# Kernel optimization log

Measured on AMD Instinct MI355X. Metric: run time of the kernel, lower is better.

## Reference

```python
import jax, jax.numpy as jnp
import numpy as np

N = 20000      # nodes
E = 320000     # edges (avg degree 16)
S = 2          # extra feature axis (mean-pooled before fc)
IN = 128       # in_feats
H = 246        # n_hidden (must be 246 to match fc = Linear(246, 1))


def setup_inputs() -> dict:
    key = jax.random.key(0)
    ks = jax.random.split(key, 8)
    feat = jax.random.normal(ks[0], (N, S, IN), jnp.float32)
    src = jax.random.randint(ks[1], (E,), 0, N, jnp.int32)
    dst = jax.random.randint(ks[2], (E,), 0, N, jnp.int32)
    glorot = lambda k, shp, fan: jax.random.normal(k, shp, jnp.float32) / np.sqrt(fan).astype(np.float32)
    return {
        "features": feat,
        "src": src,
        "dst": dst,
        "W0": glorot(ks[3], (IN, H), IN), "b0": jnp.zeros((H,), jnp.float32),
        "W1": glorot(ks[4], (H, H), H),   "b1": jnp.zeros((H,), jnp.float32),
        "W2": glorot(ks[5], (H, H), H),   "b2": jnp.zeros((H,), jnp.float32),
        "fc_w": glorot(ks[6], (H, 1), H), "fc_b": jnp.zeros((1,), jnp.float32),
    }


def reference(features, src, dst, W0, b0, W1, b1, W2, b2, fc_w, fc_b):
    # DGL GraphConv, norm='both': h' = act( D_in^{-1/2} A D_out^{-1/2} h W + b )
    ones = jnp.ones((src.shape[0],), jnp.float32)
    out_deg = jax.ops.segment_sum(ones, src, num_segments=N)
    in_deg = jax.ops.segment_sum(ones, dst, num_segments=N)
    norm_out = jax.lax.rsqrt(jnp.maximum(out_deg, 1.0))[:, None, None]  # [N,1,1]
    norm_in = jax.lax.rsqrt(jnp.maximum(in_deg, 1.0))[:, None, None]

    def graph_conv(h, W, b):
        h = h * norm_out                                      # [N,S,F] scale by src-side norm
        agg = jax.ops.segment_sum(h[src], dst, num_segments=N)  # gather->scatter-add over edges
        agg = agg * norm_in
        return jax.nn.relu(agg @ W + b)

    h = graph_conv(features.astype(jnp.float32), W0, b0)
    # dropout between layers is identity in eval mode
    h = graph_conv(h, W1, b1)
    h = graph_conv(h, W2, b2)
    return h.mean(axis=1) @ fc_w + fc_b  # [N,1]
```

## Files before the change

kernel.cpp:

```cpp
#include <hip/hip_runtime.h>
#include <hip/hip_fp16.h>

#define NN 20000
#define NE 320000
#define SS 2
#define FIN 128
#define FH 246

typedef _Float16 f16x8 __attribute__((ext_vector_type(8)));
typedef float f32x4 __attribute__((ext_vector_type(4)));

__global__ void degree_kernel(const int* __restrict__ src, const int* __restrict__ dst,
                              int* __restrict__ deg_out, int* __restrict__ deg_in) {
    int e = blockIdx.x * blockDim.x + threadIdx.x;
    if (e < NE) {
        atomicAdd(&deg_out[src[e]], 1);
        atomicAdd(&deg_in[dst[e]], 1);
    }
}

__global__ void alloc_kernel(const int* __restrict__ deg_out, const int* __restrict__ deg_in,
                             float* __restrict__ norm_out, float* __restrict__ norm_in,
                             int* __restrict__ row_start, int* __restrict__ cursor,
                             int* __restrict__ counter) {
    __shared__ int smem[256];
    __shared__ int base_s;
    int tid = threadIdx.x;
    int i = blockIdx.x * 256 + tid;
    int v  = (i < NN) ? deg_in[i] : 0;
    int vp = (v + 3) & ~3;
    smem[tid] = vp;
    __syncthreads();
    for (int off = 1; off < 256; off <<= 1) {
        int t = (tid >= off) ? smem[tid - off] : 0;
        __syncthreads();
        smem[tid] += t;
        __syncthreads();
    }
    int incl = smem[tid];
    if (tid == 0) base_s = atomicAdd(counter, smem[255]);
    __syncthreads();
    if (i < NN) {
        int excl = base_s + incl - vp;
        row_start[i] = excl;
        cursor[i]    = excl;
        norm_out[i] = rsqrtf(fmaxf((float)deg_out[i], 1.0f));
        norm_in[i]  = rsqrtf(fmaxf((float)v, 1.0f));
    }
}

__global__ void scatter_kernel(const int* __restrict__ src, const int* __restrict__ dst,
                               int* __restrict__ cursor, ushort* __restrict__ sorted_src) {
    int e = blockIdx.x * blockDim.x + threadIdx.x;
    if (e < NE) {
        int d = dst[e];
        int pos = atomicAdd(&cursor[d], 1);
        sorted_src[pos] = (ushort)src[e];
    }
}

__global__ void pad_fill(const int* __restrict__ row_start, const int* __restrict__ deg_in,
                         ushort* __restrict__ sorted_src) {
    int n = blockIdx.x * 256 + threadIdx.x;
    if (n < NN) {
        int d = deg_in[n];
        int beg = row_start[n] + d;
        int end = row_start[n] + ((d + 3) & ~3);
        for (int p = beg; p < end; ++p) sorted_src[p] = (ushort)NN;
    }
}

__global__ void convert_w_all(const float* __restrict__ W0, const float* __restrict__ W1,
                              const float* __restrict__ W2,
                              ushort* __restrict__ Wh0, ushort* __restrict__ Wl0,
                              ushort* __restrict__ Wh1, ushort* __restrict__ Wl1,
                              ushort* __restrict__ Wh2, ushort* __restrict__ Wl2) {
    int n = blockIdx.x, k = threadIdx.x;
    const float* W; ushort* Wh; ushort* Wl; int K;
    if (blockIdx.y == 0)      { W = W0; Wh = Wh0; Wl = Wl0; K = FIN; }
    else if (blockIdx.y == 1) { W = W1; Wh = Wh1; Wl = Wl1; K = FH; }
    else                      { W = W2; Wh = Wh2; Wl = Wl2; K = FH; }
    float v = (k < K && n < 246) ? W[k * 246 + n] : 0.f;
    _Float16 h = (_Float16)v;
    _Float16 l = (_Float16)(v - (float)h);
    Wh[n * 256 + k] = *(ushort*)&h;
    Wl[n * 256 + k] = *(ushort*)&l;
}

__global__ void init_out(float* __restrict__ out, const float* __restrict__ fcb,
                         float* __restrict__ norm_out) {
    int i = blockIdx.x * 256 + threadIdx.x;
    if (i < NN) out[i] = fcb[0];
    if (i == 0) norm_out[NN] = 0.f;
}

template<int F4ROW, int NCH, bool NORM>
__global__ void aggregate4(const float* __restrict__ h,
                           const int* __restrict__ row_start,
                           const int* __restrict__ deg_in,
                           const ushort* __restrict__ sorted_src,
                           const float* __restrict__ norm_out,
                           const float* __restrict__ norm_in,
                           ushort* __restrict__ Ah, ushort* __restrict__ Al) {
    int g  = threadIdx.x >> 4;
    int l  = threadIdx.x & 15;
    int cb = blockIdx.x & (NCH - 1);
    int nb = blockIdx.x / NCH;
    int n  = nb * 8 + g;
    if (n >= NN) return;
    int idx = cb * 16 + l;
    const float4* hv = (const float4*)h;
    int beg = row_start[n];
    int end = beg + ((deg_in[n] + 3) & ~3);
    float4 acc = {0.f, 0.f, 0.f, 0.f};
    for (int i = beg; i < end; i += 4) {
        ushort4 ss = *(const ushort4*)&sorted_src[i];
        int s0 = ss.x, s1 = ss.y, s2 = ss.z, s3 = ss.w;
        if (NORM) {
            float n0 = norm_out[s0], n1 = norm_out[s1];
            float n2 = norm_out[s2], n3 = norm_out[s3];
            float4 v0 = hv[(size_t)(s0 < NN ? s0 : NN - 1) * F4ROW + idx];
            float4 v1 = hv[(size_t)(s1 < NN ? s1 : NN - 1) * F4ROW + idx];
            float4 v2 = hv[(size_t)(s2 < NN ? s2 : NN - 1) * F4ROW + idx];
            float4 v3 = hv[(size_t)(s3 < NN ? s3 : NN - 1) * F4ROW + idx];
            acc.x += v0.x * n0 + v1.x * n1 + v2.x * n2 + v3.x * n3;
            acc.y += v0.y * n0 + v1.y * n1 + v2.y * n2 + v3.y * n3;
            acc.z += v0.z * n0 + v1.z * n1 + v2.z * n2 + v3.z * n3;
            acc.w += v0.w * n0 + v1.w * n1 + v2.w * n2 + v3.w * n3;
        } else {
            float4 v0 = hv[(size_t)s0 * F4ROW + idx];
            float4 v1 = hv[(size_t)s1 * F4ROW + idx];
            float4 v2 = hv[(size_t)s2 * F4ROW + idx];
            float4 v3 = hv[(size_t)s3 * F4ROW + idx];
            acc.x += v0.x + v1.x + v2.x + v3.x;
            acc.y += v0.y + v1.y + v2.y + v3.y;
            acc.z += v0.z + v1.z + v2.z + v3.z;
            acc.w += v0.w + v1.w + v2.w + v3.w;
        }
    }
    float ni = norm_in[n];
    float v[4] = {acc.x * ni, acc.y * ni, acc.z * ni, acc.w * ni};
    ushort hp[4], lp[4];
#pragma unroll
    for (int j = 0; j < 4; ++j) {
        _Float16 hh = (_Float16)v[j];
        _Float16 ll = (_Float16)(v[j] - (float)hh);
        hp[j] = *(ushort*)&hh;
        lp[j] = *(ushort*)&ll;
    }
    ((uint2*)Ah)[(size_t)n * F4ROW + idx] = *(uint2*)hp;
    ((uint2*)Al)[(size_t)n * F4ROW + idx] = *(uint2*)lp;
}

template<int KP, bool FUSE>
__global__ __launch_bounds__(256) void gemm_split(const ushort* __restrict__ Ah,
                                                  const ushort* __restrict__ Al,
                                                  const ushort* __restrict__ Wh,
                                                  const ushort* __restrict__ Wl,
                                                  const float* __restrict__ b,
                                                  void* __restrict__ outv,
                                                  const float* __restrict__ fcw,
                                                  const float* __restrict__ nrm) {
    constexpr int NT = KP / 32;
    constexpr int AS = KP / 8;
    __shared__ __align__(16) _Float16 Ah_s[64][40];
    __shared__ __align__(16) _Float16 Al_s[64][40];
    __shared__ __align__(16) _Float16 Bh_s[128][40];
    __shared__ __align__(16) _Float16 Bl_s[128][40];

    int tid  = threadIdx.x;
    int m0   = blockIdx.x * 64;
    int n0   = blockIdx.y * 128;
    int wave = tid >> 6, lane = tid & 63;
    int wm = wave >> 1, wn = wave & 1;
    int lr = lane & 15, quad = lane >> 4;

    f32x4 acc[2][4];
#pragma unroll
    for (int mi = 0; mi < 2; ++mi)
#pragma unroll
        for (int ni = 0; ni < 4; ++ni) acc[mi][ni] = {0.f, 0.f, 0.f, 0.f};

    int ar = tid >> 2;
    int aq = tid & 3;
    const uint4* Ahv = (const uint4*)Ah;
    const uint4* Alv = (const uint4*)Al;
    const uint4* Whv = (const uint4*)Wh;
    const uint4* Wlv = (const uint4*)Wl;

    for (int t0 = 0; t0 < NT; ++t0) {
        size_t abase = (size_t)(m0 + ar) * AS + t0 * 4 + aq;
        *(uint4*)&Ah_s[ar][aq * 8] = Ahv[abase];
        *(uint4*)&Al_s[ar][aq * 8] = Alv[abase];
#pragma unroll
        for (int it = 0; it < 2; ++it) {
            int f = it * 256 + tid;
            int rn = f >> 2, q = f & 3;
            size_t base = (size_t)(n0 + rn) * 32 + t0 * 4 + q;
            *(uint4*)&Bh_s[rn][q * 8] = Whv[base];
            *(uint4*)&Bl_s[rn][q * 8] = Wlv[base];
        }
        __syncthreads();

        f16x8 ah[2], al[2], bh[4], bl[4];
#pragma unroll
        for (int mi = 0; mi < 2; ++mi) {
            ah[mi] = *(const f16x8*)&Ah_s[wm * 32 + mi * 16 + lr][quad * 8];
            al[mi] = *(const f16x8*)&Al_s[wm * 32 + mi * 16 + lr][quad * 8];
        }
#pragma unroll
        for (int ni = 0; ni < 4; ++ni) {
            bh[ni] = *(const f16x8*)&Bh_s[wn * 64 + ni * 16 + lr][quad * 8];
            bl[ni] = *(const f16x8*)&Bl_s[wn * 64 + ni * 16 + lr][quad * 8];
        }
#pragma unroll
        for (int mi = 0; mi < 2; ++mi)
#pragma unroll
            for (int ni = 0; ni < 4; ++ni) {
                acc[mi][ni] = __builtin_amdgcn_mfma_f32_16x16x32_f16(ah[mi], bh[ni], acc[mi][ni], 0, 0, 0);
                acc[mi][ni] = __builtin_amdgcn_mfma_f32_16x16x32_f16(al[mi], bh[ni], acc[mi][ni], 0, 0, 0);
                acc[mi][ni] = __builtin_amdgcn_mfma_f32_16x16x32_f16(ah[mi], bl[ni], acc[mi][ni], 0, 0, 0);
            }
        __syncthreads();
    }

    if (FUSE) {
        float* out = (float*)outv;
#pragma unroll
        for (int mi = 0; mi < 2; ++mi) {
#pragma unroll
            for (int i = 0; i < 4; ++i) {
                float p = 0.f;
#pragma unroll
                for (int ni = 0; ni < 4; ++ni) {
                    int c = n0 + wn * 64 + ni * 16 + lr;
                    if (c < 246)
                        p += fmaxf(acc[mi][ni][i] + b[c], 0.f) * fcw[c];
                }
#pragma unroll
                for (int off = 8; off > 0; off >>= 1)
                    p += __shfl_down(p, off, 16);
                if (lr == 0) {
                    int m = m0 + wm * 32 + mi * 16 + quad * 4 + i;
                    atomicAdd(&out[m >> 1], 0.5f * p);
                }
            }
        }
    } else {
        float* outF = (float*)outv;
#pragma unroll
        for (int ni = 0; ni < 4; ++ni) {
            int c = n0 + wn * 64 + ni * 16 + lr;
            float bj = (c < 246) ? b[c] : 0.f;
#pragma unroll
            for (int mi = 0; mi < 2; ++mi)
#pragma unroll
                for (int i = 0; i < 4; ++i) {
                    int m = m0 + wm * 32 + mi * 16 + quad * 4 + i;
                    float no = nrm[m >> 1];
                    outF[(size_t)m * 256 + c] = fmaxf(acc[mi][ni][i] + bj, 0.f) * no;
                }
        }
    }
}

extern "C" void kernel_launch(void* const* d_in, const int* in_sizes, int n_in,
                              void* d_out, int out_size, void* d_ws, size_t ws_size,
                              hipStream_t stream) {
    const float* feat = (const float*)d_in[0];
    const int*   src  = (const int*)d_in[1];
    const int*   dst  = (const int*)d_in[2];
    const float* W0   = (const float*)d_in[3];
    const float* b0   = (const float*)d_in[4];
    const float* W1   = (const float*)d_in[5];
    const float* b1   = (const float*)d_in[6];
    const float* W2   = (const float*)d_in[7];
    const float* b2   = (const float*)d_in[8];
    const float* fcw  = (const float*)d_in[9];
    const float* fcb  = (const float*)d_in[10];
    float* out = (float*)d_out;

    char* ws = (char*)d_ws;
    size_t off = 0;
    auto alloc = [&](size_t bytes) {
        void* p = ws + off;
        off = (off + bytes + 255) & ~(size_t)255;
        return p;
    };
    int*    deg_out_i = (int*)alloc((2 * NN + 64) * sizeof(int));
    int*    deg_in_i  = deg_out_i + NN;
    int*    counter   = deg_out_i + 2 * NN;
    int*    row_start = (int*)alloc(NN * sizeof(int));
    int*    cursor    = (int*)alloc(NN * sizeof(int));
    ushort* sorted    = (ushort*)alloc((NE + 3 * NN + 16) * sizeof(ushort));
    float*  norm_out  = (float*)alloc((NN + 1) * sizeof(float));
    float*  norm_in   = (float*)alloc(NN * sizeof(float));
    ushort* Wh0 = (ushort*)alloc(256 * 256 * sizeof(ushort));
    ushort* Wl0 = (ushort*)alloc(256 * 256 * sizeof(ushort));
    ushort* Wh1 = (ushort*)alloc(256 * 256 * sizeof(ushort));
    ushort* Wl1 = (ushort*)alloc(256 * 256 * sizeof(ushort));
    ushort* Wh2 = (ushort*)alloc(256 * 256 * sizeof(ushort));
    ushort* Wl2 = (ushort*)alloc(256 * 256 * sizeof(ushort));
    ushort* Ahb = (ushort*)alloc((size_t)NN * SS * 256 * sizeof(ushort));
    ushort* Alb = (ushort*)alloc((size_t)NN * SS * 256 * sizeof(ushort));
    float*  bufH = (float*)alloc(((size_t)NN * SS * 256 + 512) * sizeof(float));

    hipMemsetAsync(deg_out_i, 0, (2 * NN + 1) * sizeof(int), stream);
    hipMemsetAsync(bufH + (size_t)NN * 512, 0, 512 * sizeof(float), stream);

    degree_kernel<<<(NE + 255) / 256, 256, 0, stream>>>(src, dst, deg_out_i, deg_in_i);
    alloc_kernel<<<(NN + 255) / 256, 256, 0, stream>>>(deg_out_i, deg_in_i, norm_out, norm_in,
                                                       row_start, cursor, counter);
    pad_fill<<<(NN + 255) / 256, 256, 0, stream>>>(row_start, deg_in_i, sorted);
    scatter_kernel<<<(NE + 255) / 256, 256, 0, stream>>>(src, dst, cursor, sorted);

    convert_w_all<<<dim3(256, 3), 256, 0, stream>>>(W0, W1, W2, Wh0, Wl0, Wh1, Wl1, Wh2, Wl2);
    init_out<<<(NN + 255) / 256, 256, 0, stream>>>(out, fcb, norm_out);

    const int NB8 = (NN + 7) / 8;
    dim3 ggrid(NN * SS / 64, 2);

    aggregate4<64, 4, true><<<NB8 * 4, 128, 0, stream>>>(feat, row_start, deg_in_i, sorted,
                                                         norm_out, norm_in, Ahb, Alb);
    gemm_split<FIN, false><<<ggrid, 256, 0, stream>>>(Ahb, Alb, Wh0, Wl0, b0, bufH, fcw, norm_out);

    aggregate4<128, 8, false><<<NB8 * 8, 128, 0, stream>>>(bufH, row_start, deg_in_i, sorted,
                                                           norm_out, norm_in, Ahb, Alb);
    gemm_split<256, false><<<ggrid, 256, 0, stream>>>(Ahb, Alb, Wh1, Wl1, b1, bufH, fcw, norm_out);

    aggregate4<128, 8, false><<<NB8 * 8, 128, 0, stream>>>(bufH, row_start, deg_in_i, sorted,
                                                           norm_out, norm_in, Ahb, Alb);
    gemm_split<256, true><<<ggrid, 256, 0, stream>>>(Ahb, Alb, Wh2, Wl2, b2, out, fcw, norm_out);
}
```

Measured before the change: 355.2 us.

## Enlarge GEMM M-tile to 128, prefetch edge indices, nontemporal aggregate stores

The split-fp16 GEMM tile grows from 64x128 to 128x128 per block, so each wave computes a 64x64 sub-tile. This improves reuse of the loaded W tiles and halves the grid in M, with bounds checks and zero-padded A buffers to cover the ragged last tile. The aggregation loop now prefetches the next ushort4 of source indices one iteration ahead, and writes its hi/lo fp16 outputs with nontemporal stores. The costs are more accumulator registers and LDS per block, which may lower occupancy, plus four extra memsets.

```diff
diff --git a/kernel.cpp b/kernel.cpp
--- a/kernel.cpp
+++ b/kernel.cpp
@@ -113,9 +113,12 @@
     int beg = row_start[n];
     int end = beg + ((deg_in[n] + 3) & ~3);
     float4 acc = {0.f, 0.f, 0.f, 0.f};
+    ushort4 ss;
+    if (beg < end) ss = *(const ushort4*)&sorted_src[beg];
     for (int i = beg; i < end; i += 4) {
-        ushort4 ss = *(const ushort4*)&sorted_src[i];
-        int s0 = ss.x, s1 = ss.y, s2 = ss.z, s3 = ss.w;
+        ushort4 cur = ss;
+        if (i + 4 < end) ss = *(const ushort4*)&sorted_src[i + 4];
+        int s0 = cur.x, s1 = cur.y, s2 = cur.z, s3 = cur.w;
         if (NORM) {
             float n0 = norm_out[s0], n1 = norm_out[s1];
             float n2 = norm_out[s2], n3 = norm_out[s3];
@@ -148,8 +151,11 @@
         hp[j] = *(ushort*)&hh;
         lp[j] = *(ushort*)&ll;
     }
-    ((uint2*)Ah)[(size_t)n * F4ROW + idx] = *(uint2*)hp;
-    ((uint2*)Al)[(size_t)n * F4ROW + idx] = *(uint2*)lp;
+    unsigned long long hv64, lv64;
+    __builtin_memcpy(&hv64, hp, 8);
+    __builtin_memcpy(&lv64, lp, 8);
+    __builtin_nontemporal_store(hv64, (unsigned long long*)Ah + (size_t)n * F4ROW + idx);
+    __builtin_nontemporal_store(lv64, (unsigned long long*)Al + (size_t)n * F4ROW + idx);
 }
 
 template<int KP, bool FUSE>
@@ -163,50 +169,48 @@
                                                   const float* __restrict__ nrm) {
     constexpr int NT = KP / 32;
     constexpr int AS = KP / 8;
-    __shared__ __align__(16) _Float16 Ah_s[64][40];
-    __shared__ __align__(16) _Float16 Al_s[64][40];
+    __shared__ __align__(16) _Float16 Ah_s[128][40];
+    __shared__ __align__(16) _Float16 Al_s[128][40];
     __shared__ __align__(16) _Float16 Bh_s[128][40];
     __shared__ __align__(16) _Float16 Bl_s[128][40];
 
     int tid  = threadIdx.x;
-    int m0   = blockIdx.x * 64;
+    int m0   = blockIdx.x * 128;
     int n0   = blockIdx.y * 128;
     int wave = tid >> 6, lane = tid & 63;
     int wm = wave >> 1, wn = wave & 1;
     int lr = lane & 15, quad = lane >> 4;
 
-    f32x4 acc[2][4];
-#pragma unroll
-    for (int mi = 0; mi < 2; ++mi)
+    f32x4 acc[4][4];
+#pragma unroll
+    for (int mi = 0; mi < 4; ++mi)
 #pragma unroll
         for (int ni = 0; ni < 4; ++ni) acc[mi][ni] = {0.f, 0.f, 0.f, 0.f};
 
-    int ar = tid >> 2;
-    int aq = tid & 3;
     const uint4* Ahv = (const uint4*)Ah;
     const uint4* Alv = (const uint4*)Al;
     const uint4* Whv = (const uint4*)Wh;
     const uint4* Wlv = (const uint4*)Wl;
 
     for (int t0 = 0; t0 < NT; ++t0) {
-        size_t abase = (size_t)(m0 + ar) * AS + t0 * 4 + aq;
-        *(uint4*)&Ah_s[ar][aq * 8] = Ahv[abase];
-        *(uint4*)&Al_s[ar][aq * 8] = Alv[abase];
 #pragma unroll
         for (int it = 0; it < 2; ++it) {
             int f = it * 256 + tid;
             int rn = f >> 2, q = f & 3;
-            size_t base = (size_t)(n0 + rn) * 32 + t0 * 4 + q;
-            *(uint4*)&Bh_s[rn][q * 8] = Whv[base];
-            *(uint4*)&Bl_s[rn][q * 8] = Wlv[base];
+            size_t abase = (size_t)(m0 + rn) * AS + t0 * 4 + q;
+            *(uint4*)&Ah_s[rn][q * 8] = Ahv[abase];
+            *(uint4*)&Al_s[rn][q * 8] = Alv[abase];
+            size_t bbase = (size_t)(n0 + rn) * 32 + t0 * 4 + q;
+            *(uint4*)&Bh_s[rn][q * 8] = Whv[bbase];
+            *(uint4*)&Bl_s[rn][q * 8] = Wlv[bbase];
         }
         __syncthreads();
 
-        f16x8 ah[2], al[2], bh[4], bl[4];
-#pragma unroll
-        for (int mi = 0; mi < 2; ++mi) {
-            ah[mi] = *(const f16x8*)&Ah_s[wm * 32 + mi * 16 + lr][quad * 8];
-            al[mi] = *(const f16x8*)&Al_s[wm * 32 + mi * 16 + lr][quad * 8];
+        f16x8 ah[4], al[4], bh[4], bl[4];
+#pragma unroll
+        for (int mi = 0; mi < 4; ++mi) {
+            ah[mi] = *(const f16x8*)&Ah_s[wm * 64 + mi * 16 + lr][quad * 8];
+            al[mi] = *(const f16x8*)&Al_s[wm * 64 + mi * 16 + lr][quad * 8];
         }
 #pragma unroll
         for (int ni = 0; ni < 4; ++ni) {
@@ -214,7 +218,7 @@
             bl[ni] = *(const f16x8*)&Bl_s[wn * 64 + ni * 16 + lr][quad * 8];
         }
 #pragma unroll
-        for (int mi = 0; mi < 2; ++mi)
+        for (int mi = 0; mi < 4; ++mi)
 #pragma unroll
             for (int ni = 0; ni < 4; ++ni) {
                 acc[mi][ni] = __builtin_amdgcn_mfma_f32_16x16x32_f16(ah[mi], bh[ni], acc[mi][ni], 0, 0, 0);
@@ -227,7 +231,7 @@
     if (FUSE) {
         float* out = (float*)outv;
 #pragma unroll
-        for (int mi = 0; mi < 2; ++mi) {
+        for (int mi = 0; mi < 4; ++mi) {
 #pragma unroll
             for (int i = 0; i < 4; ++i) {
                 float p = 0.f;
@@ -240,10 +244,9 @@
 #pragma unroll
                 for (int off = 8; off > 0; off >>= 1)
                     p += __shfl_down(p, off, 16);
-                if (lr == 0) {
-                    int m = m0 + wm * 32 + mi * 16 + quad * 4 + i;
+                int m = m0 + wm * 64 + mi * 16 + quad * 4 + i;
+                if (lr == 0 && m < NN * SS)
                     atomicAdd(&out[m >> 1], 0.5f * p);
-                }
             }
         }
     } else {
@@ -253,12 +256,14 @@
             int c = n0 + wn * 64 + ni * 16 + lr;
             float bj = (c < 246) ? b[c] : 0.f;
 #pragma unroll
-            for (int mi = 0; mi < 2; ++mi)
+            for (int mi = 0; mi < 4; ++mi)
 #pragma unroll
                 for (int i = 0; i < 4; ++i) {
-                    int m = m0 + wm * 32 + mi * 16 + quad * 4 + i;
-                    float no = nrm[m >> 1];
-                    outF[(size_t)m * 256 + c] = fmaxf(acc[mi][ni][i] + bj, 0.f) * no;
+                    int m = m0 + wm * 64 + mi * 16 + quad * 4 + i;
+                    if (m < NN * SS) {
+                        float no = nrm[m >> 1];
+                        outF[(size_t)m * 256 + c] = fmaxf(acc[mi][ni][i] + bj, 0.f) * no;
+                    }
                 }
         }
     }
@@ -301,12 +306,16 @@
     ushort* Wl1 = (ushort*)alloc(256 * 256 * sizeof(ushort));
     ushort* Wh2 = (ushort*)alloc(256 * 256 * sizeof(ushort));
     ushort* Wl2 = (ushort*)alloc(256 * 256 * sizeof(ushort));
-    ushort* Ahb = (ushort*)alloc((size_t)NN * SS * 256 * sizeof(ushort));
-    ushort* Alb = (ushort*)alloc((size_t)NN * SS * 256 * sizeof(ushort));
+    ushort* Ahb = (ushort*)alloc((size_t)(NN * SS + 64) * 256 * sizeof(ushort));
+    ushort* Alb = (ushort*)alloc((size_t)(NN * SS + 64) * 256 * sizeof(ushort));
     float*  bufH = (float*)alloc(((size_t)NN * SS * 256 + 512) * sizeof(float));
 
     hipMemsetAsync(deg_out_i, 0, (2 * NN + 1) * sizeof(int), stream);
     hipMemsetAsync(bufH + (size_t)NN * 512, 0, 512 * sizeof(float), stream);
+    hipMemsetAsync(Ahb + (size_t)NN * SS * 128, 0, 64 * 128 * sizeof(ushort), stream);
+    hipMemsetAsync(Alb + (size_t)NN * SS * 128, 0, 64 * 128 * sizeof(ushort), stream);
+    hipMemsetAsync(Ahb + (size_t)NN * SS * 256, 0, 64 * 256 * sizeof(ushort), stream);
+    hipMemsetAsync(Alb + (size_t)NN * SS * 256, 0, 64 * 256 * sizeof(ushort), stream);
 
     degree_kernel<<<(NE + 255) / 256, 256, 0, stream>>>(src, dst, deg_out_i, deg_in_i);
     alloc_kernel<<<(NN + 255) / 256, 256, 0, stream>>>(deg_out_i, deg_in_i, norm_out, norm_in,
@@ -318,7 +327,8 @@
     init_out<<<(NN + 255) / 256, 256, 0, stream>>>(out, fcb, norm_out);
 
     const int NB8 = (NN + 7) / 8;
-    dim3 ggrid(NN * SS / 64, 2);
+    const int GX  = (NN * SS + 127) / 128;
+    dim3 ggrid(GX, 2);
 
     aggregate4<64, 4, true><<<NB8 * 4, 128, 0, stream>>>(feat, row_start, deg_in_i, sorted,
                                                          norm_out, norm_in, Ahb, Alb);
```

Measured after the change: 391.8 us. 10.3% more time.
